# Kernel optimization log

Measured on AMD Instinct MI355X. Metric: run time of the kernel, lower is better.

## Reference

```python
import jax, jax.numpy as jnp
import numpy as np
from jax import lax

B, NM, P, F, E, H, K = 32, 131072, 256, 3, 64, 4, 3
DH = E // H


def layer_norm(x, gamma, beta, eps=1e-5):
    mu = x.mean(-1, keepdims=True)
    var = ((x - mu) ** 2).mean(-1, keepdims=True)
    return (x - mu) * lax.rsqrt(var + eps) * gamma + beta


def knn_interp(x, pos_x, pos_y, k=K):
    """x: [B, Nx, F] features at pos_x [Nx, 2]; interpolate to pos_y [Ny, 2].
    Positions are shared across the batch (they are tiled in the torch code),
    so KNN indices/weights are computed once. Matches torch knn + inverse-
    squared-distance weighted scatter (uniform per-batch counts => gather form).
    """
    d2 = jnp.sum((pos_y[:, None, :] - pos_x[None, :, :]) ** 2, axis=-1)  # [Ny, Nx]
    neg_d2, idx = lax.top_k(-d2, k)                                      # [Ny, k]
    w = 1.0 / jnp.clip(-neg_d2, 1e-16)                                   # [Ny, k]
    w = lax.stop_gradient(w)  # torch computes weights under no_grad
    gathered = x[:, idx, :]                                              # [B, Ny, k, F]
    num = jnp.sum(gathered * w[None, :, :, None], axis=2)                # [B, Ny, F]
    den = jnp.sum(w, axis=1)[None, :, None]                              # [1, Ny, 1]
    return num / den


def setup_inputs() -> dict:
    key = jax.random.key(0)
    ks = jax.random.split(key, 8)
    return {
        "node_attr": jax.random.normal(ks[0], (B * NM, F), jnp.float32),
        "position_mesh": jax.random.uniform(ks[1], (NM, 2), jnp.float32),
        "position_pivotal": jax.random.uniform(ks[2], (P, 2), jnp.float32),
        "ln_gamma": jnp.ones((F,), jnp.float32),
        "ln_beta": jnp.zeros((F,), jnp.float32),
        "Wf": jax.random.normal(ks[3], (E, F), jnp.float32) * (2.0 / E) ** 0.5,
        "bf": jnp.zeros((E,), jnp.float32),
        "Wp": jax.random.normal(ks[4], (E, 2), jnp.float32) * (2.0 / E) ** 0.5,
        "bp": jnp.zeros((E,), jnp.float32),
        "in_proj_w": jax.random.normal(ks[5], (3 * E, E), jnp.float32) * (1.0 / E) ** 0.5,
        "in_proj_b": jnp.zeros((3 * E,), jnp.float32),
        "batch_size": B,
    }


def reference(node_attr, position_mesh, position_pivotal, ln_gamma, ln_beta,
              Wf, bf, Wp, bp, in_proj_w, in_proj_b, batch_size):
    x = node_attr.reshape(batch_size, -1, F)                 # [B, NM, F]
    # PivotalNorm after encoder (encoder/decoder MeshGraphNet omitted: undefined dep)
    x = layer_norm(x, ln_gamma, ln_beta)
    # ---- downsample: mesh -> pivotal via inverse-distance KNN interpolation ----
    y = knn_interp(x, position_mesh, position_pivotal)       # [B, P, F]
    # attention-based pooling over pivotal nodes
    q = (jnp.einsum('bpf,ef->bpe', y, Wf) + bf
         + (position_pivotal @ Wp.T + bp)[None])             # [B, P, E]
    Wq, Wk = in_proj_w[:E], in_proj_w[E:2 * E]
    bq, bk = in_proj_b[:E], in_proj_b[E:2 * E]
    Q = (q @ Wq.T + bq).reshape(batch_size, P, H, DH)
    Kt = (q @ Wk.T + bk).reshape(batch_size, P, H, DH)
    scores = jnp.einsum('bqhd,bkhd->bhqk', Q, Kt) / np.float32(np.sqrt(DH))
    attn = jax.nn.softmax(scores, axis=-1)                   # [B, H, P, P]
    attn_w = attn.mean(axis=1)                               # avg heads, [B, P, P]
    y = jnp.einsum('bqk,bkf->bqf', attn_w, y)                # [B, P, F]
    # ---- interpolate: pivotal -> mesh ----
    out = knn_interp(y, position_pivotal, position_mesh)     # [B, NM, F]
    return out.reshape(-1, F)
```

## Files before the change

kernel.cpp:

```cpp
#include <hip/hip_runtime.h>
#include <math.h>

#define NM 131072
#define PP 256
#define BB 32
#define INF_F 3.0e38f

#define GM   64
#define GM2  (GM * GM)
#define CAPM 96
#define GP   16
#define GP2  (GP * GP)
#define CAPP 8

typedef unsigned long long u64;

__device__ __forceinline__ u64 packkey(float d, int i) {
  return ((u64)__float_as_uint(d) << 32) | (unsigned)i;
}

__device__ __forceinline__ void ins3k(u64 k, u64& k0, u64& k1, u64& k2) {
  bool l0 = k < k0, l1 = k < k1, l2 = k < k2;
  k2 = l1 ? k1 : (l2 ? k : k2);
  k1 = l0 ? k0 : (l1 ? k : k1);
  k0 = l0 ? k : k0;
}

__device__ __forceinline__ float dist2(float ax, float ay, float bx, float by) {
  float dx = ax - bx, dy = ay - by;
  return __fadd_rn(__fmul_rn(dx, dx), __fmul_rn(dy, dy));
}

__global__ __launch_bounds__(256)
void build_buckets(const float* __restrict__ mesh, const float* __restrict__ piv,
                   unsigned* __restrict__ cntM, unsigned* __restrict__ cntP,
                   unsigned* __restrict__ ovfc,
                   float* __restrict__ bufM,
                   int* __restrict__ bufP,
                   float* __restrict__ ovfM, int* __restrict__ ovfP,
                   float* __restrict__ y2) {
  const int g = blockIdx.x * 256 + threadIdx.x;
  if (g < NM) {
    float2 mp = ((const float2*)mesh)[g];
    int cx = min((int)(mp.x * GM), GM - 1);
    int cy = min((int)(mp.y * GM), GM - 1);
    int c = cy * GM + cx;
    unsigned s = atomicAdd(&cntM[c], 1u);
    if (s < CAPM) {
      float* d = bufM + (size_t)(c * CAPM + s) * 3;
      d[0] = mp.x; d[1] = mp.y; ((int*)d)[2] = g;
    } else {
      unsigned o = atomicAdd(&ovfc[0], 1u);
      float* d = ovfM + (size_t)o * 3;
      d[0] = mp.x; d[1] = mp.y; ((int*)d)[2] = g;
    }
  }
  if (blockIdx.x == 0 && threadIdx.x < PP) {
    const int p = threadIdx.x;
    float2 pv = ((const float2*)piv)[p];
    int cx = min((int)(pv.x * GP), GP - 1);
    int cy = min((int)(pv.y * GP), GP - 1);
    int c = cy * GP + cx;
    unsigned s = atomicAdd(&cntP[c], 1u);
    if (s < CAPP) bufP[c * CAPP + s] = p;
    else { unsigned o = atomicAdd(&ovfc[1], 1u); ovfP[o] = p; }
  }
  if (blockIdx.x == 1) {
    for (int j = threadIdx.x; j < BB * PP * 3; j += 256) y2[j] = 0.f;
  }
}

__global__ __launch_bounds__(256)
void knnA_grid(const float* __restrict__ piv,
               const unsigned* __restrict__ cntM, const float* __restrict__ bufM,
               const unsigned* __restrict__ ovfc, const float* __restrict__ ovfM,
               float* __restrict__ wA, int* __restrict__ idxA) {
  const int p = blockIdx.x;
  const int t = threadIdx.x;
  __shared__ u64 sk[256 * 3];
  __shared__ u64 g3[3];
  __shared__ int sdone;

  const float2 pv = ((const float2*)piv)[p];
  const int cx = min((int)(pv.x * GM), GM - 1);
  const int cy = min((int)(pv.y * GM), GM - 1);

  u64 b0 = ~0ull, b1 = ~0ull, b2 = ~0ull;

  {
    int x0 = max(cx - 1, 0), x1 = min(cx + 1, GM - 1);
    int y0 = max(cy - 1, 0), y1 = min(cy + 1, GM - 1);
    for (int yy = y0; yy <= y1; ++yy) {
      int cb = yy * GM + x0;
      int tot = (x1 - x0 + 1) * CAPM;
      for (int s = t; s < tot; s += 256) {
        int ci = s / CAPM, j = s - ci * CAPM;
        int c = cb + ci;
        if (j < (int)min(cntM[c], (unsigned)CAPM)) {
          const float* cp = bufM + (size_t)(c * CAPM + j) * 3;
          float d = dist2(pv.x, pv.y, cp[0], cp[1]);
          ins3k(packkey(d, ((const int*)cp)[2]), b0, b1, b2);
        }
      }
    }
    int no = (int)ovfc[0];
    for (int j = t; j < no; j += 256) {
      const float* cp = ovfM + (size_t)j * 3;
      float d = dist2(pv.x, pv.y, cp[0], cp[1]);
      ins3k(packkey(d, ((const int*)cp)[2]), b0, b1, b2);
    }
  }

  int R = 1;
  u64 p0 = ~0ull, p1 = ~0ull, p2 = ~0ull;
  while (true) {
    sk[t * 3 + 0] = b0; sk[t * 3 + 1] = b1; sk[t * 3 + 2] = b2;
    __syncthreads();
    if (t < 32) {
      u64 e0 = ~0ull, e1 = ~0ull, e2 = ~0ull;
#pragma unroll
      for (int s = 0; s < 8; ++s) {
        int o = (t + 32 * s) * 3;
        ins3k(sk[o], e0, e1, e2); ins3k(sk[o + 1], e0, e1, e2); ins3k(sk[o + 2], e0, e1, e2);
      }
      sk[t * 3] = e0; sk[t * 3 + 1] = e1; sk[t * 3 + 2] = e2;
    }
    __syncthreads();
    if (t == 0) {
      u64 e0 = p0, e1 = p1, e2 = p2;
      for (int s = 0; s < 32; ++s) {
        ins3k(sk[s * 3], e0, e1, e2); ins3k(sk[s * 3 + 1], e0, e1, e2); ins3k(sk[s * 3 + 2], e0, e1, e2);
      }
      g3[0] = e0; g3[1] = e1; g3[2] = e2;
      float d2f = __uint_as_float((unsigned)(e2 >> 32));
      float md = (float)R * (1.0f / GM);
      sdone = (md * md > d2f) ? 1 : 0;
    }
    __syncthreads();
    if (sdone) break;
    p0 = g3[0]; p1 = g3[1]; p2 = g3[2];
    b0 = b1 = b2 = ~0ull;
    R += 1;
    int x0 = max(cx - R, 0), x1 = min(cx + R, GM - 1);
    for (int pass = 0; pass < 2; ++pass) {
      int yy = pass ? cy + R : cy - R;
      if (yy < 0 || yy > GM - 1) continue;
      int cb = yy * GM + x0;
      int tot = (x1 - x0 + 1) * CAPM;
      for (int s = t; s < tot; s += 256) {
        int ci = s / CAPM, j = s - ci * CAPM;
        int c = cb + ci;
        if (j < (int)min(cntM[c], (unsigned)CAPM)) {
          const float* cp = bufM + (size_t)(c * CAPM + j) * 3;
          float d = dist2(pv.x, pv.y, cp[0], cp[1]);
          ins3k(packkey(d, ((const int*)cp)[2]), b0, b1, b2);
        }
      }
    }
    int yy0 = max(cy - R + 1, 0), yy1 = min(cy + R - 1, GM - 1);
    for (int pass = 0; pass < 2; ++pass) {
      int xx = pass ? cx + R : cx - R;
      if (xx < 0 || xx > GM - 1) continue;
      int tot = (yy1 - yy0 + 1) * CAPM;
      for (int s = t; s < tot; s += 256) {
        int ri = s / CAPM, j = s - ri * CAPM;
        int c = (yy0 + ri) * GM + xx;
        if (j < (int)min(cntM[c], (unsigned)CAPM)) {
          const float* cp = bufM + (size_t)(c * CAPM + j) * 3;
          float d = dist2(pv.x, pv.y, cp[0], cp[1]);
          ins3k(packkey(d, ((const int*)cp)[2]), b0, b1, b2);
        }
      }
    }
    __syncthreads();
  }
  if (t == 0) {
#pragma unroll
    for (int k = 0; k < 3; ++k) {
      u64 e = g3[k];
      float d = __uint_as_float((unsigned)(e >> 32));
      wA[p * 3 + k] = 1.0f / fmaxf(d, 1e-16f);
      idxA[p * 3 + k] = (int)(unsigned)(e & 0xffffffffu);
    }
  }
}

__global__ __launch_bounds__(128, 2)
void gather_qqk(const float* __restrict__ node, const float* __restrict__ piv,
                const float* __restrict__ gamma, const float* __restrict__ beta,
                const float* __restrict__ Wf, const float* __restrict__ bf,
                const float* __restrict__ Wp, const float* __restrict__ bp,
                const float* __restrict__ ipw, const float* __restrict__ ipb,
                const float* __restrict__ wA, const int* __restrict__ idxA,
                float* __restrict__ y, float* __restrict__ Qh, float* __restrict__ Kh) {
  const int b = blockIdx.x >> 5;
  const int ptile = (blockIdx.x & 31) * 8;
  const int t = threadIdx.x;
  __shared__ float qs[8][64];
  __shared__ float ys[8][3];

  if (t < 8) {
    const int p = ptile + t;
    const float g0 = gamma[0], g1 = gamma[1], g2 = gamma[2];
    const float be0 = beta[0], be1 = beta[1], be2 = beta[2];
    float num0 = 0.f, num1 = 0.f, num2 = 0.f, den = 0.f;
#pragma unroll
    for (int k = 0; k < 3; ++k) {
      int idx = idxA[p * 3 + k];
      float w = wA[p * 3 + k];
      const float* r = node + ((size_t)b * NM + idx) * 3;
      float a0 = r[0], a1 = r[1], a2 = r[2];
      float mu = (a0 + a1 + a2) * (1.0f / 3.0f);
      float e0 = a0 - mu, e1 = a1 - mu, e2 = a2 - mu;
      float var = (e0 * e0 + e1 * e1 + e2 * e2) * (1.0f / 3.0f);
      float sc = 1.0f / sqrtf(var + 1e-5f);
      num0 += (e0 * sc * g0 + be0) * w;
      num1 += (e1 * sc * g1 + be1) * w;
      num2 += (e2 * sc * g2 + be2) * w;
      den += w;
    }
    float o0 = num0 / den, o1 = num1 / den, o2 = num2 / den;
    ys[t][0] = o0; ys[t][1] = o1; ys[t][2] = o2;
    float* yr = y + (b * PP + p) * 3;
    yr[0] = o0; yr[1] = o1; yr[2] = o2;
  }
  __syncthreads();

  const int e = t & 63;
  const int half = t >> 6;
  {
    float wf0 = Wf[e * 3], wf1 = Wf[e * 3 + 1], wf2 = Wf[e * 3 + 2];
    float wp0 = Wp[e * 2], wp1 = Wp[e * 2 + 1];
    float cst = bf[e] + bp[e];
    for (int r = half; r < 8; r += 2) {
      int p = ptile + r;
      float pe = piv[2 * p] * wp0 + piv[2 * p + 1] * wp1;
      qs[r][e] = ys[r][0] * wf0 + ys[r][1] * wf1 + ys[r][2] * wf2 + cst + pe;
    }
  }
  __syncthreads();

  const int row = half * 64 + e;
  float wreg[64];
  const float4* W4 = (const float4*)(ipw + row * 64);
#pragma unroll
  for (int j = 0; j < 16; ++j) {
    float4 v = W4[j];
    wreg[4 * j] = v.x; wreg[4 * j + 1] = v.y; wreg[4 * j + 2] = v.z; wreg[4 * j + 3] = v.w;
  }
  float bias = ipb[row];
  float* dst = half ? Kh : Qh;
  const int h = e >> 4, d = e & 15;
  for (int r = 0; r < 8; ++r) {
    float acc = bias;
#pragma unroll
    for (int j = 0; j < 64; ++j) acc += qs[r][j] * wreg[j];
    int p = ptile + r;
    dst[(((b * 4 + h) * PP) + p) * 16 + d] = acc;
  }
}

__global__ void attn_kernel(const float* __restrict__ Qh, const float* __restrict__ Kh,
                            const float* __restrict__ y, float* __restrict__ y2) {
  const int b = blockIdx.x >> 3;
  const int h = (blockIdx.x >> 1) & 3;
  const int qh = blockIdx.x & 1;
  const int t = threadIdx.x;
  const int q = qh * 128 + t;

  __shared__ float Ks[PP * 16];
  __shared__ float ys[PP * 3];
  {
    const float4* src = (const float4*)(Kh + (size_t)(b * 4 + h) * PP * 16);
    float4* dst = (float4*)Ks;
#pragma unroll
    for (int j = 0; j < 8; ++j) dst[j * 128 + t] = src[j * 128 + t];
    const float* ysrc = y + b * PP * 3;
#pragma unroll
    for (int j = 0; j < 6; ++j) ys[j * 128 + t] = ysrc[j * 128 + t];
  }
  __syncthreads();

  const float4* q4 = (const float4*)(Qh + ((size_t)((b * 4 + h) * PP) + q) * 16);
  float4 qa = q4[0], qb = q4[1], qc = q4[2], qd = q4[3];

  float m0 = -INF_F, m1 = -INF_F, m2 = -INF_F, m3 = -INF_F;
  float l0 = 0, l1 = 0, l2 = 0, l3 = 0;
  float a00 = 0, a01 = 0, a02 = 0, a10 = 0, a11 = 0, a12 = 0;
  float a20 = 0, a21 = 0, a22 = 0, a30 = 0, a31 = 0, a32 = 0;

#define CHAIN(c, mC, lC, aC0, aC1, aC2) { \
    int k = (c) * 64 + kk; \
    const float4* kr = (const float4*)(Ks + k * 16); \
    float4 K0 = kr[0], K1 = kr[1], K2 = kr[2], K3 = kr[3]; \
    float dot = qa.x*K0.x + qa.y*K0.y + qa.z*K0.z + qa.w*K0.w \
              + qb.x*K1.x + qb.y*K1.y + qb.z*K1.z + qb.w*K1.w \
              + qc.x*K2.x + qc.y*K2.y + qc.z*K2.z + qc.w*K2.w \
              + qd.x*K3.x + qd.y*K3.y + qd.z*K3.z + qd.w*K3.w; \
    float s = dot * 0.25f; \
    float mn = fmaxf(mC, s); \
    float pE = __expf(s - mn); \
    float sc = __expf(mC - mn); \
    float yv0 = ys[k * 3], yv1 = ys[k * 3 + 1], yv2 = ys[k * 3 + 2]; \
    lC = lC * sc + pE; \
    aC0 = aC0 * sc + pE * yv0; \
    aC1 = aC1 * sc + pE * yv1; \
    aC2 = aC2 * sc + pE * yv2; \
    mC = mn; }

#pragma unroll 2
  for (int kk = 0; kk < 64; ++kk) {
    CHAIN(0, m0, l0, a00, a01, a02)
    CHAIN(1, m1, l1, a10, a11, a12)
    CHAIN(2, m2, l2, a20, a21, a22)
    CHAIN(3, m3, l3, a30, a31, a32)
  }
#undef CHAIN

  float M = fmaxf(fmaxf(m0, m1), fmaxf(m2, m3));
  float e0 = __expf(m0 - M), e1 = __expf(m1 - M), e2 = __expf(m2 - M), e3 = __expf(m3 - M);
  float l = l0 * e0 + l1 * e1 + l2 * e2 + l3 * e3;
  float A0 = a00 * e0 + a10 * e1 + a20 * e2 + a30 * e3;
  float A1 = a01 * e0 + a11 * e1 + a21 * e2 + a31 * e3;
  float A2 = a02 * e0 + a12 * e1 + a22 * e2 + a32 * e3;
  float inv = 0.25f / l;
  float* o = y2 + (b * PP + q) * 3;
  atomicAdd(o + 0, A0 * inv);
  atomicAdd(o + 1, A1 * inv);
  atomicAdd(o + 2, A2 * inv);
}

__global__ __launch_bounds__(256)
void interp_knnB_out(const float* __restrict__ mesh, const float* __restrict__ piv,
                     const unsigned* __restrict__ cntP, const int* __restrict__ bufP,
                     const unsigned* __restrict__ ovfc, const int* __restrict__ ovfP,
                     const float* __restrict__ y2, float* __restrict__ out) {
  const int t = threadIdx.x;
  __shared__ float spx[PP], spy[PP];
  __shared__ unsigned scnt[GP2];
  __shared__ int sbuf[GP2 * CAPP];
  {
    float2 pvv = ((const float2*)piv)[t];
    spx[t] = pvv.x; spy[t] = pvv.y;
    scnt[t] = cntP[t];
    for (int j = t; j < GP2 * CAPP; j += 256) sbuf[j] = bufP[j];
  }
  __syncthreads();

  const int m = blockIdx.x * 256 + t;
  const float2 mv = ((const float2*)mesh)[m];
  const int cx = min((int)(mv.x * GP), GP - 1);
  const int cy = min((int)(mv.y * GP), GP - 1);
  u64 k0 = ~0ull, k1 = ~0ull, k2 = ~0ull;

  {
    int x0 = max(cx - 2, 0), x1 = min(cx + 2, GP - 1);
    int y0 = max(cy - 2, 0), y1 = min(cy + 2, GP - 1);
    for (int yy = y0; yy <= y1; ++yy)
      for (int xx = x0; xx <= x1; ++xx) {
        int c = yy * GP + xx;
        int n = (int)min(scnt[c], (unsigned)CAPP);
        for (int j = 0; j < n; ++j) {
          int qq = sbuf[c * CAPP + j];
          float d = dist2(mv.x, mv.y, spx[qq], spy[qq]);
          ins3k(packkey(d, qq), k0, k1, k2);
        }
      }
    int no = (int)ovfc[1];
    for (int j = 0; j < no; ++j) {
      int qq = ovfP[j];
      float d = dist2(mv.x, mv.y, spx[qq], spy[qq]);
      ins3k(packkey(d, qq), k0, k1, k2);
    }
  }
  int R = 2;
  while (true) {
    float d2f = __uint_as_float((unsigned)(k2 >> 32));
    float md = (float)R * (1.0f / GP);
    if (md * md > d2f) break;
    R += 1;
    if (R >= 2 * GP) break;
    int x0 = max(cx - R, 0), x1 = min(cx + R, GP - 1);
    for (int pass = 0; pass < 2; ++pass) {
      int yy = pass ? cy + R : cy - R;
      if (yy < 0 || yy > GP - 1) continue;
      for (int xx = x0; xx <= x1; ++xx) {
        int c = yy * GP + xx;
        int n = (int)min(scnt[c], (unsigned)CAPP);
        for (int j = 0; j < n; ++j) {
          int qq = sbuf[c * CAPP + j];
          float d = dist2(mv.x, mv.y, spx[qq], spy[qq]);
          ins3k(packkey(d, qq), k0, k1, k2);
        }
      }
    }
    int yy0 = max(cy - R + 1, 0), yy1 = min(cy + R - 1, GP - 1);
    for (int pass = 0; pass < 2; ++pass) {
      int xx = pass ? cx + R : cx - R;
      if (xx < 0 || xx > GP - 1) continue;
      for (int yy = yy0; yy <= yy1; ++yy) {
        int c = yy * GP + xx;
        int n = (int)min(scnt[c], (unsigned)CAPP);
        for (int j = 0; j < n; ++j) {
          int qq = sbuf[c * CAPP + j];
          float d = dist2(mv.x, mv.y, spx[qq], spy[qq]);
          ins3k(packkey(d, qq), k0, k1, k2);
        }
      }
    }
  }

  float d0 = __uint_as_float((unsigned)(k0 >> 32));
  float d1 = __uint_as_float((unsigned)(k1 >> 32));
  float d2v = __uint_as_float((unsigned)(k2 >> 32));
  int j0 = (int)(unsigned)(k0 & 0xffffffffu) * 3;
  int j1 = (int)(unsigned)(k1 & 0xffffffffu) * 3;
  int j2 = (int)(unsigned)(k2 & 0xffffffffu) * 3;
  float w0 = 1.0f / fmaxf(d0, 1e-16f);
  float w1 = 1.0f / fmaxf(d1, 1e-16f);
  float w2 = 1.0f / fmaxf(d2v, 1e-16f);
  float inv = 1.0f / (w0 + w1 + w2);

  for (int b = 0; b < BB; ++b) {
    const float* yb = y2 + b * PP * 3;
    float3 r0 = *(const float3*)(yb + j0);
    float3 r1 = *(const float3*)(yb + j1);
    float3 r2 = *(const float3*)(yb + j2);
    float3 res;
    res.x = (w0 * r0.x + w1 * r1.x + w2 * r2.x) * inv;
    res.y = (w0 * r0.y + w1 * r1.y + w2 * r2.y) * inv;
    res.z = (w0 * r0.z + w1 * r1.z + w2 * r2.z) * inv;
    *(float3*)(out + ((size_t)b * NM + m) * 3) = res;
  }
}

extern "C" void kernel_launch(void* const* d_in, const int* in_sizes, int n_in,
                              void* d_out, int out_size, void* d_ws, size_t ws_size,
                              hipStream_t stream) {
  const float* node  = (const float*)d_in[0];
  const float* mesh  = (const float*)d_in[1];
  const float* piv   = (const float*)d_in[2];
  const float* gamma = (const float*)d_in[3];
  const float* beta  = (const float*)d_in[4];
  const float* Wf    = (const float*)d_in[5];
  const float* bf    = (const float*)d_in[6];
  const float* Wp    = (const float*)d_in[7];
  const float* bp    = (const float*)d_in[8];
  const float* ipw   = (const float*)d_in[9];
  const float* ipb   = (const float*)d_in[10];
  float* out = (float*)d_out;

  unsigned* cntM = (unsigned*)d_ws;
  unsigned* cntP = cntM + 4096;
  unsigned* ovfc = cntP + 256;
  float* bufM = (float*)d_ws + 4608;
  int*   bufP = (int*)(bufM + (size_t)GM2 * CAPM * 3);
  float* ovfM = (float*)(bufP + GP2 * CAPP);
  int*   ovfP = (int*)(ovfM + (size_t)NM * 3);
  float* wA   = (float*)(ovfP + PP);
  int*   idxA = (int*)(wA + PP * 3);
  float* y    = (float*)(idxA + PP * 3);
  float* Qh   = y + BB * PP * 3;
  float* Kh   = Qh + BB * PP * 64;
  float* y2   = Kh + BB * PP * 64;

  hipMemsetAsync(cntM, 0, 4608 * sizeof(unsigned), stream);
  build_buckets<<<NM / 256, 256, 0, stream>>>(mesh, piv, cntM, cntP, ovfc,
                                              bufM, bufP, ovfM, ovfP, y2);
  knnA_grid<<<PP, 256, 0, stream>>>(piv, cntM, bufM, ovfc, ovfM, wA, idxA);
  gather_qqk<<<BB * 32, 128, 0, stream>>>(node, piv, gamma, beta, Wf, bf, Wp, bp, ipw, ipb,
                                          wA, idxA, y, Qh, Kh);
  attn_kernel<<<BB * 4 * 2, 128, 0, stream>>>(Qh, Kh, y, y2);
  interp_knnB_out<<<NM / 256, 256, 0, stream>>>(mesh, piv, cntP, bufP, ovfc, ovfP, y2, out);
}
```

Baseline: 220.4 us.

## Split attention keys across 8 lanes per query pair and merge by shuffle

The attention kernel goes from 128 threads per block, one query each and four serial key chains, to 512 threads where 8 lanes share two queries. Each lane processes a strided subset of 32 keys, and the partial online-softmax states are merged with xor shuffles. K rows are padded to a 5-float4 stride and y is packed into float4 to cut LDS bank conflicts. This raises parallelism in a small grid of 256 blocks at the cost of extra shuffle and exp work in the merge.

```diff
diff --git a/kernel.cpp b/kernel.cpp
--- a/kernel.cpp
+++ b/kernel.cpp
@@ -260,74 +260,101 @@
   }
 }
 
-__global__ void attn_kernel(const float* __restrict__ Qh, const float* __restrict__ Kh,
-                            const float* __restrict__ y, float* __restrict__ y2) {
+__global__ __launch_bounds__(512, 2)
+void attn_kernel(const float* __restrict__ Qh, const float* __restrict__ Kh,
+                 const float* __restrict__ y, float* __restrict__ y2) {
   const int b = blockIdx.x >> 3;
   const int h = (blockIdx.x >> 1) & 3;
   const int qh = blockIdx.x & 1;
   const int t = threadIdx.x;
-  const int q = qh * 128 + t;
-
-  __shared__ float Ks[PP * 16];
-  __shared__ float ys[PP * 3];
+  const int sub = t & 7;
+  const int rt = t >> 3;
+
+  __shared__ float4 sK[PP * 5];
+  __shared__ float4 sY[PP];
+
   {
     const float4* src = (const float4*)(Kh + (size_t)(b * 4 + h) * PP * 16);
-    float4* dst = (float4*)Ks;
-#pragma unroll
-    for (int j = 0; j < 8; ++j) dst[j * 128 + t] = src[j * 128 + t];
-    const float* ysrc = y + b * PP * 3;
-#pragma unroll
-    for (int j = 0; j < 6; ++j) ys[j * 128 + t] = ysrc[j * 128 + t];
+#pragma unroll
+    for (int i = t; i < PP * 4; i += 512) {
+      int k = i >> 2, j = i & 3;
+      sK[k * 5 + j] = src[i];
+    }
+    if (t < PP) {
+      const float* yr = y + (b * PP + t) * 3;
+      sY[t] = make_float4(yr[0], yr[1], yr[2], 0.f);
+    }
   }
   __syncthreads();
 
-  const float4* q4 = (const float4*)(Qh + ((size_t)((b * 4 + h) * PP) + q) * 16);
-  float4 qa = q4[0], qb = q4[1], qc = q4[2], qd = q4[3];
-
-  float m0 = -INF_F, m1 = -INF_F, m2 = -INF_F, m3 = -INF_F;
-  float l0 = 0, l1 = 0, l2 = 0, l3 = 0;
-  float a00 = 0, a01 = 0, a02 = 0, a10 = 0, a11 = 0, a12 = 0;
-  float a20 = 0, a21 = 0, a22 = 0, a30 = 0, a31 = 0, a32 = 0;
-
-#define CHAIN(c, mC, lC, aC0, aC1, aC2) { \
-    int k = (c) * 64 + kk; \
-    const float4* kr = (const float4*)(Ks + k * 16); \
-    float4 K0 = kr[0], K1 = kr[1], K2 = kr[2], K3 = kr[3]; \
-    float dot = qa.x*K0.x + qa.y*K0.y + qa.z*K0.z + qa.w*K0.w \
-              + qb.x*K1.x + qb.y*K1.y + qb.z*K1.z + qb.w*K1.w \
-              + qc.x*K2.x + qc.y*K2.y + qc.z*K2.z + qc.w*K2.w \
-              + qd.x*K3.x + qd.y*K3.y + qd.z*K3.z + qd.w*K3.w; \
-    float s = dot * 0.25f; \
-    float mn = fmaxf(mC, s); \
-    float pE = __expf(s - mn); \
-    float sc = __expf(mC - mn); \
-    float yv0 = ys[k * 3], yv1 = ys[k * 3 + 1], yv2 = ys[k * 3 + 2]; \
-    lC = lC * sc + pE; \
-    aC0 = aC0 * sc + pE * yv0; \
-    aC1 = aC1 * sc + pE * yv1; \
-    aC2 = aC2 * sc + pE * yv2; \
-    mC = mn; }
-
-#pragma unroll 2
-  for (int kk = 0; kk < 64; ++kk) {
-    CHAIN(0, m0, l0, a00, a01, a02)
-    CHAIN(1, m1, l1, a10, a11, a12)
-    CHAIN(2, m2, l2, a20, a21, a22)
-    CHAIN(3, m3, l3, a30, a31, a32)
-  }
-#undef CHAIN
-
-  float M = fmaxf(fmaxf(m0, m1), fmaxf(m2, m3));
-  float e0 = __expf(m0 - M), e1 = __expf(m1 - M), e2 = __expf(m2 - M), e3 = __expf(m3 - M);
-  float l = l0 * e0 + l1 * e1 + l2 * e2 + l3 * e3;
-  float A0 = a00 * e0 + a10 * e1 + a20 * e2 + a30 * e3;
-  float A1 = a01 * e0 + a11 * e1 + a21 * e2 + a31 * e3;
-  float A2 = a02 * e0 + a12 * e1 + a22 * e2 + a32 * e3;
-  float inv = 0.25f / l;
-  float* o = y2 + (b * PP + q) * 3;
-  atomicAdd(o + 0, A0 * inv);
-  atomicAdd(o + 1, A1 * inv);
-  atomicAdd(o + 2, A2 * inv);
+  const int q0 = qh * 128 + rt * 2;
+  const float4* q4 = (const float4*)(Qh + ((size_t)((b * 4 + h) * PP) + q0) * 16);
+  float4 A0 = q4[0], A1 = q4[1], A2 = q4[2], A3 = q4[3];
+  float4 B0 = q4[4], B1 = q4[5], B2 = q4[6], B3 = q4[7];
+
+  float m0 = -INF_F, l0 = 0.f, x0 = 0.f, x1 = 0.f, x2 = 0.f;
+  float m1 = -INF_F, l1 = 0.f, z0 = 0.f, z1 = 0.f, z2 = 0.f;
+
+#pragma unroll 4
+  for (int kk = 0; kk < 32; ++kk) {
+    int k = kk * 8 + sub;
+    float4 K0 = sK[k * 5 + 0], K1 = sK[k * 5 + 1], K2 = sK[k * 5 + 2], K3 = sK[k * 5 + 3];
+    float4 yv = sY[k];
+    float s0 = (A0.x*K0.x + A0.y*K0.y + A0.z*K0.z + A0.w*K0.w
+              + A1.x*K1.x + A1.y*K1.y + A1.z*K1.z + A1.w*K1.w
+              + A2.x*K2.x + A2.y*K2.y + A2.z*K2.z + A2.w*K2.w
+              + A3.x*K3.x + A3.y*K3.y + A3.z*K3.z + A3.w*K3.w) * 0.25f;
+    float s1 = (B0.x*K0.x + B0.y*K0.y + B0.z*K0.z + B0.w*K0.w
+              + B1.x*K1.x + B1.y*K1.y + B1.z*K1.z + B1.w*K1.w
+              + B2.x*K2.x + B2.y*K2.y + B2.z*K2.z + B2.w*K2.w
+              + B3.x*K3.x + B3.y*K3.y + B3.z*K3.z + B3.w*K3.w) * 0.25f;
+    {
+      float mn = fmaxf(m0, s0);
+      float p = __expf(s0 - mn), sc = __expf(m0 - mn);
+      l0 = l0 * sc + p;
+      x0 = x0 * sc + p * yv.x; x1 = x1 * sc + p * yv.y; x2 = x2 * sc + p * yv.z;
+      m0 = mn;
+    }
+    {
+      float mn = fmaxf(m1, s1);
+      float p = __expf(s1 - mn), sc = __expf(m1 - mn);
+      l1 = l1 * sc + p;
+      z0 = z0 * sc + p * yv.x; z1 = z1 * sc + p * yv.y; z2 = z2 * sc + p * yv.z;
+      m1 = mn;
+    }
+  }
+
+#pragma unroll
+  for (int off = 1; off < 8; off <<= 1) {
+    float mo = __shfl_xor(m0, off), lo = __shfl_xor(l0, off);
+    float b0 = __shfl_xor(x0, off), b1 = __shfl_xor(x1, off), b2 = __shfl_xor(x2, off);
+    float M = fmaxf(m0, mo);
+    float es = __expf(m0 - M), eo = __expf(mo - M);
+    l0 = l0 * es + lo * eo;
+    x0 = x0 * es + b0 * eo; x1 = x1 * es + b1 * eo; x2 = x2 * es + b2 * eo;
+    m0 = M;
+
+    float mo1 = __shfl_xor(m1, off), lo1 = __shfl_xor(l1, off);
+    float c0 = __shfl_xor(z0, off), c1 = __shfl_xor(z1, off), c2 = __shfl_xor(z2, off);
+    float M1 = fmaxf(m1, mo1);
+    float es1 = __expf(m1 - M1), eo1 = __expf(mo1 - M1);
+    l1 = l1 * es1 + lo1 * eo1;
+    z0 = z0 * es1 + c0 * eo1; z1 = z1 * es1 + c1 * eo1; z2 = z2 * es1 + c2 * eo1;
+    m1 = M1;
+  }
+
+  if (sub == 0) {
+    float inv0 = 0.25f / l0;
+    float inv1 = 0.25f / l1;
+    float* o0 = y2 + (b * PP + q0) * 3;
+    atomicAdd(o0 + 0, x0 * inv0);
+    atomicAdd(o0 + 1, x1 * inv0);
+    atomicAdd(o0 + 2, x2 * inv0);
+    float* o1 = o0 + 3;
+    atomicAdd(o1 + 0, z0 * inv1);
+    atomicAdd(o1 + 1, z1 * inv1);
+    atomicAdd(o1 + 2, z2 * inv1);
+  }
 }
 
 __global__ __launch_bounds__(256)
@@ -470,6 +497,6 @@
   knnA_grid<<<PP, 256, 0, stream>>>(piv, cntM, bufM, ovfc, ovfM, wA, idxA);
   gather_qqk<<<BB * 32, 128, 0, stream>>>(node, piv, gamma, beta, Wf, bf, Wp, bp, ipw, ipb,
                                           wA, idxA, y, Qh, Kh);
-  attn_kernel<<<BB * 4 * 2, 128, 0, stream>>>(Qh, Kh, y, y2);
+  attn_kernel<<<BB * 4 * 2, 512, 0, stream>>>(Qh, Kh, y, y2);
   interp_knnB_out<<<NM / 256, 256, 0, stream>>>(mesh, piv, cntP, bufP, ovfc, ovfP, y2, out);
 }
```

Result: faster. 192.3 us (-12.7%).
